# Performance work log

Measured on AMD Instinct MI355X. Metric: run time of the kernel, lower is better.

The kernel has to match this reference:

```python
import jax, jax.numpy as jnp
import numpy as np

B, C, H, L, P = 64, 64, 256, 64, 32
N_REAL = 2047
N = N_REAL + 1  # slot 0 is the null-child zero vector


def setup_inputs() -> dict:
    key = jax.random.key(0)
    ks = jax.random.split(key, 8)
    return {
        "node_feats": jax.random.normal(ks[0], (B, C, N), jnp.float32),
        "z": jax.random.normal(ks[1], (B, L), jnp.float32),
        "children": jax.random.randint(ks[2], (B, 3 * N_REAL), 0, N, jnp.int32),
        "conv1_w": jax.random.normal(ks[3], (H, C, 3), jnp.float32) * 0.05,
        "conv1_b": jnp.zeros((H,), jnp.float32),
        "conv2_w": jax.random.normal(ks[4], (H, H, 3), jnp.float32) * 0.05,
        "conv2_b": jnp.zeros((H,), jnp.float32),
        "mlp_w1": jax.random.normal(ks[5], (H + L, H), jnp.float32) * 0.05,
        "mlp_b1": jnp.zeros((H,), jnp.float32),
        "mlp_w2": jax.random.normal(ks[6], (H, P), jnp.float32) * 0.05,
        "mlp_b2": jnp.zeros((P,), jnp.float32),
    }


def _tree_conv(x, children, w, b):
    # x: [B, Cin, N]; children: [B, 3*N_real] indices of (self,left,right) triples
    g = jax.vmap(lambda xb, ib: xb[:, ib])(x, children)      # [B, Cin, 3*N_real]
    g = g.reshape(g.shape[0], g.shape[1], -1, 3)             # [B, Cin, N_real, 3]
    out = jnp.einsum('bcnk,hck->bhn', g, w) + b[None, :, None]  # Conv1d k=3 s=3
    zero = jnp.zeros((out.shape[0], out.shape[1], 1), out.dtype)
    return jnp.concatenate([zero, out], axis=2)              # [B, Cout, N]


def _tree_norm(x):
    # TreeLayerNorm: normalize each tree over all (channel, node) elements
    mean = jnp.mean(x, axis=(1, 2), keepdims=True)
    std = jnp.std(x, axis=(1, 2), keepdims=True, ddof=1)  # torch.std is unbiased
    return (x - mean) / (std + 1e-5)


def reference(node_feats, z, children, conv1_w, conv1_b, conv2_w, conv2_b,
              mlp_w1, mlp_b1, mlp_w2, mlp_b2):
    x = _tree_conv(node_feats, children, conv1_w, conv1_b)
    x = jax.nn.relu(_tree_norm(x))
    x = _tree_conv(x, children, conv2_w, conv2_b)
    x = jax.nn.relu(_tree_norm(x))                           # [B, H, N]
    z_exp = jnp.broadcast_to(z[:, :, None], (z.shape[0], z.shape[1], x.shape[2]))
    xz = jnp.concatenate([x, z_exp], axis=1)                 # [B, H+L, N]
    xz = xz.transpose(0, 2, 1)                               # [B, N, H+L]
    h = jax.nn.relu(xz @ mlp_w1 + mlp_b1)                    # [B, N, H]
    return h @ mlp_w2 + mlp_b2                               # [B, N, P]
```

## Files before the change

### kernel.cpp

```cpp
#include <hip/hip_runtime.h>
#include <hip/hip_bf16.h>

#define BATCH 64
#define CC    64
#define HH    256
#define LL    64
#define PP    32
#define NREAL 2047
#define NN    2048
#define MTOT  (HH*NN)

typedef unsigned short u16;
typedef __attribute__((ext_vector_type(8))) short short8;
typedef __attribute__((ext_vector_type(4))) float f32x4;

__device__ __forceinline__ float bu2f(u16 u) {
    return __uint_as_float(((unsigned)u) << 16);
}
__device__ __forceinline__ u16 f2bu(float f) {
    __hip_bfloat16 h = __float2bfloat16(f);
    return *reinterpret_cast<u16*>(&h);
}
__device__ __forceinline__ float ldv(const void* p, long long i, int f32) {
    return f32 ? ((const float*)p)[i] : bu2f(((const u16*)p)[i]);
}

__device__ __forceinline__ void swz(int id, int& b, int& tile) {
    b    = (id & 7) + 8 * ((id >> 3) & 7);
    tile = id >> 6;
}

__global__ __launch_bounds__(256) void detect_k(const u16* __restrict__ nf,
                                                int* __restrict__ flag) {
    __shared__ int cnt;
    if (threadIdx.x == 0) cnt = 0;
    __syncthreads();
    int c = 0;
#pragma unroll
    for (int i = 0; i < 16; ++i) {
        unsigned u = nf[threadIdx.x * 16 + i];
        unsigned e = (u >> 7) & 0xFF;
        if (e >= 161) c++;
    }
    atomicAdd(&cnt, c);
    __syncthreads();
    if (threadIdx.x == 0) flag[0] = (cnt > 64) ? 1 : 0;
}

__global__ __launch_bounds__(256) void prep_k(const void* __restrict__ c1w,
                                              const void* __restrict__ c2w,
                                              u16* __restrict__ wt1m,
                                              u16* __restrict__ wt2m,
                                              u16* __restrict__ x1t,
                                              float* __restrict__ statsz,
                                              const int* __restrict__ flag) {
    int isF32 = flag[0];
    int blk = blockIdx.x, tid = threadIdx.x;
    if (blk < 960) {
        const void* w = (blk < 192) ? c1w : c2w;
        u16* dst      = (blk < 192) ? wt1m : wt2m;
        int cinShift  = (blk < 192) ? 6 : 8;
        int t = ((blk < 192) ? blk : (blk - 192)) * 256 + tid;
        int CIN = 1 << cinShift;
        int kin = t & 31;
        int rest = t >> 5;
        int h = rest & (HH - 1);
        int ks = rest >> 8;
        int k = ks * 32 + kin;
        int kk = k >> cinShift, c = k & (CIN - 1);
        dst[t] = f2bu(ldv(w, (((long long)h << cinShift) + c) * 3 + kk, isF32));
    } else {
        int b = blk - 960;
        x1t[(long long)b * NN * HH + tid] = 0;
        if (b == 0) statsz[tid] = 0.f;
    }
}

__global__ __launch_bounds__(256) void tr_nf_k(const void* __restrict__ nf,
                                               u16* __restrict__ nf_t,
                                               const int* __restrict__ flag) {
    __shared__ u16 t[64][65];
    int isF32 = flag[0];
    int b = blockIdx.y;
    int n0 = blockIdx.x * 64;
    int tid = threadIdx.x;
    int lane = tid & 63, grp = tid >> 6;
#pragma unroll
    for (int i = 0; i < 16; ++i) {
        int c = grp * 16 + i;
        float v = ldv(nf, ((long long)b * CC + c) * NN + n0 + lane, isF32);
        t[c][lane] = f2bu(v);
    }
    __syncthreads();
#pragma unroll
    for (int i = 0; i < 16; ++i) {
        int n = grp * 16 + i;
        nf_t[((long long)b * NN + n0 + n) * CC + lane] = t[lane][n];
    }
}

__global__ __launch_bounds__(256) void wmlp2_k(const void* __restrict__ mw1,
                                               const void* __restrict__ mw2,
                                               u16* __restrict__ w1m,
                                               u16* __restrict__ w2m,
                                               const int* __restrict__ flag) {
    int isF32 = flag[0];
    int blk = blockIdx.x, tid = threadIdx.x;
    const void* w = (blk < 320) ? mw1 : mw2;
    u16* dst      = (blk < 320) ? w1m : w2m;
    int colShift  = (blk < 320) ? 8 : 5;
    int t = ((blk < 320) ? blk : (blk - 320)) * 256 + tid;
    int COLS = 1 << colShift;
    int kin = t & 31;
    int rest = t >> 5;
    int col = rest & (COLS - 1);
    int ks = rest >> colShift;
    dst[t] = f2bu(ldv(w, ((long long)(ks * 32 + kin) << colShift) + col, isF32));
}

__device__ __forceinline__ void load_norm(const float* stats, int b,
                                          float& mean, float& rstd) {
    float s = stats[b * 2], ss = stats[b * 2 + 1];
    float m = s / (float)MTOT;
    float var = (ss - s * s / (float)MTOT) / (float)(MTOT - 1);
    var = fmaxf(var, 0.f);
    mean = m;
    rstd = 1.f / (sqrtf(var) + 1e-5f);
}

template<int CIN>
__global__ __launch_bounds__(512, 2) void convm_k(const u16* __restrict__ x_t,
                                                  const int* __restrict__ children,
                                                  const u16* __restrict__ wtm,
                                                  const void* __restrict__ bias,
                                                  const float* __restrict__ stats_in,
                                                  float* __restrict__ stats_out,
                                                  u16* __restrict__ out_t,
                                                  const int* __restrict__ flag) {
    constexpr int KT = CIN / 32;
    constexpr int RE = CIN + 8;
    __shared__ u16 A[2][64 * RE];
    __shared__ int cidx[192];
    __shared__ float ps[16];

    int isF32 = flag[0];
    int b, ntile;
    swz(blockIdx.x, b, ntile);
    int n0 = ntile * 64;
    int tid = threadIdx.x;
    int lane = tid & 63, w = tid >> 6;
    int l15 = lane & 15, quad = lane >> 4;

    float mean = 0.f, rstd = 1.f;
    bool donorm = (stats_in != nullptr);
    if (donorm) load_norm(stats_in, b, mean, rstd);

    const long long cbase = (long long)b * (3 * NREAL);
    if (tid < 192) {
        int gi = 3 * n0 + tid;
        cidx[tid] = (gi < 3 * NREAL) ? children[cbase + gi] : 0;
    }
    __syncthreads();

    const long long xbase = (long long)b * NN;
    const u16* wb = wtm + ((long long)(w * 32 + l15)) * 32 + quad * 8;

    if (CIN == 256) {
        uint2 g0[8];
#pragma unroll
        for (int u = 0; u < 8; ++u) {
            int nd = w * 8 + u;
            g0[u] = *(const uint2*)(x_t + (xbase + cidx[3 * nd]) * CIN + lane * 4);
        }
#pragma unroll
        for (int u = 0; u < 8; ++u) {
            int nd = w * 8 + u;
            float f[4];
            f[0] = bu2f((u16)(g0[u].x & 0xffff)); f[1] = bu2f((u16)(g0[u].x >> 16));
            f[2] = bu2f((u16)(g0[u].y & 0xffff)); f[3] = bu2f((u16)(g0[u].y >> 16));
            if (donorm) {
#pragma unroll
                for (int j = 0; j < 4; ++j) f[j] = fmaxf((f[j] - mean) * rstd, 0.f);
            }
            uint2 o;
            o.x = (unsigned)f2bu(f[0]) | ((unsigned)f2bu(f[1]) << 16);
            o.y = (unsigned)f2bu(f[2]) | ((unsigned)f2bu(f[3]) << 16);
            *(uint2*)&A[0][nd * RE + lane * 4] = o;
        }
    } else {
        uint2 g0[2];
#pragma unroll
        for (int u = 0; u < 2; ++u) {
            int nd = w * 8 + u * 4 + quad;
            g0[u] = *(const uint2*)(x_t + (xbase + cidx[3 * nd]) * CIN + l15 * 4);
        }
#pragma unroll
        for (int u = 0; u < 2; ++u) {
            int nd = w * 8 + u * 4 + quad;
            *(uint2*)&A[0][nd * RE + l15 * 4] = g0[u];
        }
    }
    __syncthreads();

    f32x4 acc[4][2];
#pragma unroll
    for (int mt = 0; mt < 4; ++mt)
#pragma unroll
        for (int nt = 0; nt < 2; ++nt) acc[mt][nt] = (f32x4){0.f, 0.f, 0.f, 0.f};

#pragma unroll
    for (int t = 0; t < 3; ++t) {
        const u16* Ac = &A[t & 1][0];
        u16* An = &A[(t + 1) & 1][0];

        short8 Bc[KT][2];
#pragma unroll
        for (int ks = 0; ks < KT; ++ks) {
            const u16* wn = wb + (long long)(t * KT + ks) * 8192;
            Bc[ks][0] = *(const short8*)(wn);
            Bc[ks][1] = *(const short8*)(wn + 512);
        }

        uint2 gv[8];
        uint2 gs[2];
        if (t < 2) {
            if (CIN == 256) {
#pragma unroll
                for (int u = 0; u < 8; ++u) {
                    int nd = w * 8 + u;
                    gv[u] = *(const uint2*)(x_t + (xbase + cidx[3 * nd + t + 1]) * CIN
                                            + lane * 4);
                }
            } else {
#pragma unroll
                for (int u = 0; u < 2; ++u) {
                    int nd = w * 8 + u * 4 + quad;
                    gs[u] = *(const uint2*)(x_t + (xbase + cidx[3 * nd + t + 1]) * CIN
                                            + l15 * 4);
                }
            }
        }

        short8 a0 = *(const short8*)&Ac[(l15)      * RE + quad * 8];
        short8 a1 = *(const short8*)&Ac[(16 + l15) * RE + quad * 8];
        short8 a2 = *(const short8*)&Ac[(32 + l15) * RE + quad * 8];
        short8 a3 = *(const short8*)&Ac[(48 + l15) * RE + quad * 8];
#pragma unroll
        for (int ks = 0; ks < KT; ++ks) {
            short8 ca0 = a0, ca1 = a1, ca2 = a2, ca3 = a3;
            if (ks + 1 < KT) {
                int ko = (ks + 1) * 32 + quad * 8;
                a0 = *(const short8*)&Ac[(l15)      * RE + ko];
                a1 = *(const short8*)&Ac[(16 + l15) * RE + ko];
                a2 = *(const short8*)&Ac[(32 + l15) * RE + ko];
                a3 = *(const short8*)&Ac[(48 + l15) * RE + ko];
            }
            acc[0][0] = __builtin_amdgcn_mfma_f32_16x16x32_bf16(ca0, Bc[ks][0], acc[0][0], 0, 0, 0);
            acc[1][0] = __builtin_amdgcn_mfma_f32_16x16x32_bf16(ca1, Bc[ks][0], acc[1][0], 0, 0, 0);
            acc[2][0] = __builtin_amdgcn_mfma_f32_16x16x32_bf16(ca2, Bc[ks][0], acc[2][0], 0, 0, 0);
            acc[3][0] = __builtin_amdgcn_mfma_f32_16x16x32_bf16(ca3, Bc[ks][0], acc[3][0], 0, 0, 0);
            acc[0][1] = __builtin_amdgcn_mfma_f32_16x16x32_bf16(ca0, Bc[ks][1], acc[0][1], 0, 0, 0);
            acc[1][1] = __builtin_amdgcn_mfma_f32_16x16x32_bf16(ca1, Bc[ks][1], acc[1][1], 0, 0, 0);
            acc[2][1] = __builtin_amdgcn_mfma_f32_16x16x32_bf16(ca2, Bc[ks][1], acc[2][1], 0, 0, 0);
            acc[3][1] = __builtin_amdgcn_mfma_f32_16x16x32_bf16(ca3, Bc[ks][1], acc[3][1], 0, 0, 0);
        }

        if (t < 2) {
            if (CIN == 256) {
#pragma unroll
                for (int u = 0; u < 8; ++u) {
                    int nd = w * 8 + u;
                    float f[4];
                    f[0] = bu2f((u16)(gv[u].x & 0xffff));
                    f[1] = bu2f((u16)(gv[u].x >> 16));
                    f[2] = bu2f((u16)(gv[u].y & 0xffff));
                    f[3] = bu2f((u16)(gv[u].y >> 16));
                    if (donorm) {
#pragma unroll
                        for (int j = 0; j < 4; ++j)
                            f[j] = fmaxf((f[j] - mean) * rstd, 0.f);
                    }
                    uint2 o;
                    o.x = (unsigned)f2bu(f[0]) | ((unsigned)f2bu(f[1]) << 16);
                    o.y = (unsigned)f2bu(f[2]) | ((unsigned)f2bu(f[3]) << 16);
                    *(uint2*)&An[nd * RE + lane * 4] = o;
                }
            } else {
#pragma unroll
                for (int u = 0; u < 2; ++u) {
                    int nd = w * 8 + u * 4 + quad;
                    *(uint2*)&An[nd * RE + l15 * 4] = gs[u];
                }
            }
        }
        __syncthreads();
    }

    float s = 0.f, ss = 0.f;
#pragma unroll
    for (int nt = 0; nt < 2; ++nt) {
        int h = w * 32 + nt * 16 + l15;
        float bv = ldv(bias, h, isF32);
#pragma unroll
        for (int mt = 0; mt < 4; ++mt) {
#pragma unroll
            for (int r = 0; r < 4; ++r) {
                int nc = n0 + mt * 16 + quad * 4 + r;
                if (nc < NREAL) {
                    float v = acc[mt][nt][r] + bv;
                    s += v;
                    ss += v * v;
                    out_t[((long long)b * NN + 1 + nc) * HH + h] = f2bu(v);
                }
            }
        }
    }
#pragma unroll
    for (int off = 32; off; off >>= 1) {
        s  += __shfl_down(s, off);
        ss += __shfl_down(ss, off);
    }
    if (lane == 0) { ps[w] = s; ps[8 + w] = ss; }
    __syncthreads();
    if (tid == 0) {
        float S = 0.f, SS = 0.f;
#pragma unroll
        for (int i = 0; i < 8; ++i) { S += ps[i]; SS += ps[8 + i]; }
        atomicAdd(&stats_out[b * 2],     S);
        atomicAdd(&stats_out[b * 2 + 1], SS);
    }
    if (CIN == 256 && ntile == 0 && tid < 32) {
        uint4 zz = {0u, 0u, 0u, 0u};
        *(uint4*)&out_t[((long long)b * NN) * HH + tid * 8] = zz;
    }
}

#define REX 328
#define REH 264
__global__ __launch_bounds__(256, 4) void mlpm_k(const u16* __restrict__ x2t,
                                                 const void* __restrict__ z,
                                                 const u16* __restrict__ w1m,
                                                 const void* __restrict__ b1,
                                                 const u16* __restrict__ w2m,
                                                 const void* __restrict__ b2,
                                                 const float* __restrict__ stats,
                                                 void* __restrict__ out,
                                                 const int* __restrict__ flag) {
    __shared__ u16 xz[32 * REX];
    __shared__ u16 hbuf[32 * REH];
    int isF32 = flag[0];
    int b, tile;
    swz(blockIdx.x, b, tile);
    int n0 = tile * 32;
    int tid = threadIdx.x;
    int lane = tid & 63, w = tid >> 6;
    int l15 = lane & 15, quad = lane >> 4;

    float mean, rstd;
    load_norm(stats, b, mean, rstd);
    u16 zb = f2bu(ldv(z, (long long)b * LL + lane, isF32));

    uint2 vv[8];
#pragma unroll
    for (int u = 0; u < 8; ++u) {
        int node = w * 8 + u;
        vv[u] = *(const uint2*)(x2t + ((long long)(b * NN + n0 + node)) * HH
                                + lane * 4);
    }
#pragma unroll
    for (int u = 0; u < 8; ++u) {
        int node = w * 8 + u;
        float f[4];
        f[0] = bu2f((u16)(vv[u].x & 0xffff));
        f[1] = bu2f((u16)(vv[u].x >> 16));
        f[2] = bu2f((u16)(vv[u].y & 0xffff));
        f[3] = bu2f((u16)(vv[u].y >> 16));
#pragma unroll
        for (int j = 0; j < 4; ++j) f[j] = fmaxf((f[j] - mean) * rstd, 0.f);
        uint2 o;
        o.x = (unsigned)f2bu(f[0]) | ((unsigned)f2bu(f[1]) << 16);
        o.y = (unsigned)f2bu(f[2]) | ((unsigned)f2bu(f[3]) << 16);
        *(uint2*)&xz[node * REX + lane * 4] = o;
        xz[node * REX + HH + lane] = zb;
    }
    __syncthreads();

    f32x4 acc[2][4];
#pragma unroll
    for (int mt = 0; mt < 2; ++mt)
#pragma unroll
        for (int nt = 0; nt < 4; ++nt) acc[mt][nt] = (f32x4){0.f, 0.f, 0.f, 0.f};

    const u16* wbase = w1m + ((long long)(w * 64 + l15)) * 32 + quad * 8;
    short8 bf0 = *(const short8*)(wbase);
    short8 bf1 = *(const short8*)(wbase + 512);
    short8 bf2 = *(const short8*)(wbase + 1024);
    short8 bf3 = *(const short8*)(wbase + 1536);
    short8 a0 = *(const short8*)&xz[l15 * REX + quad * 8];
    short8 a1 = *(const short8*)&xz[(16 + l15) * REX + quad * 8];

    for (int ks = 0; ks < 10; ++ks) {
        short8 c0 = bf0, c1 = bf1, c2 = bf2, c3 = bf3;
        short8 ca0 = a0, ca1 = a1;
        if (ks + 1 < 10) {
            const u16* wn = wbase + (long long)(ks + 1) * 8192;
            bf0 = *(const short8*)(wn);
            bf1 = *(const short8*)(wn + 512);
            bf2 = *(const short8*)(wn + 1024);
            bf3 = *(const short8*)(wn + 1536);
            a0 = *(const short8*)&xz[l15 * REX + (ks + 1) * 32 + quad * 8];
            a1 = *(const short8*)&xz[(16 + l15) * REX + (ks + 1) * 32 + quad * 8];
        }
        acc[0][0] = __builtin_amdgcn_mfma_f32_16x16x32_bf16(ca0, c0, acc[0][0], 0, 0, 0);
        acc[1][0] = __builtin_amdgcn_mfma_f32_16x16x32_bf16(ca1, c0, acc[1][0], 0, 0, 0);
        acc[0][1] = __builtin_amdgcn_mfma_f32_16x16x32_bf16(ca0, c1, acc[0][1], 0, 0, 0);
        acc[1][1] = __builtin_amdgcn_mfma_f32_16x16x32_bf16(ca1, c1, acc[1][1], 0, 0, 0);
        acc[0][2] = __builtin_amdgcn_mfma_f32_16x16x32_bf16(ca0, c2, acc[0][2], 0, 0, 0);
        acc[1][2] = __builtin_amdgcn_mfma_f32_16x16x32_bf16(ca1, c2, acc[1][2], 0, 0, 0);
        acc[0][3] = __builtin_amdgcn_mfma_f32_16x16x32_bf16(ca0, c3, acc[0][3], 0, 0, 0);
        acc[1][3] = __builtin_amdgcn_mfma_f32_16x16x32_bf16(ca1, c3, acc[1][3], 0, 0, 0);
    }
#pragma unroll
    for (int nt = 0; nt < 4; ++nt) {
        int j = w * 64 + nt * 16 + l15;
        float bv = ldv(b1, j, isF32);
#pragma unroll
        for (int mt = 0; mt < 2; ++mt)
#pragma unroll
            for (int r = 0; r < 4; ++r) {
                int node = mt * 16 + quad * 4 + r;
                hbuf[node * REH + j] = f2bu(fmaxf(acc[mt][nt][r] + bv, 0.f));
            }
    }
    __syncthreads();

    int mt = w & 1, nt = w >> 1;
    f32x4 acc2 = (f32x4){0.f, 0.f, 0.f, 0.f};
#pragma unroll
    for (int ks = 0; ks < 8; ++ks) {
        short8 a = *(const short8*)&hbuf[(mt * 16 + l15) * REH + ks * 32 + quad * 8];
        short8 bf = *(const short8*)(w2m + ((long long)ks * PP + nt * 16 + l15) * 32 + quad * 8);
        acc2 = __builtin_amdgcn_mfma_f32_16x16x32_bf16(a, bf, acc2, 0, 0, 0);
    }
    int p = nt * 16 + l15;
    float bp = ldv(b2, p, isF32);
#pragma unroll
    for (int r = 0; r < 4; ++r) {
        int node = mt * 16 + quad * 4 + r;
        long long o = ((long long)(b * NN + n0 + node)) * PP + p;
        float v = acc2[r] + bp;
        if (isF32) ((float*)out)[o] = v;
        else       ((u16*)out)[o] = f2bu(v);
    }
}

__global__ __launch_bounds__(256) void fill0_k(void* out, const int* flag, int n) {
    int i = blockIdx.x * 256 + threadIdx.x;
    if (i >= n) return;
    if (flag[0]) ((float*)out)[i] = 0.f;
    else ((u16*)out)[i] = 0;
}

extern "C" void kernel_launch(void* const* d_in, const int* in_sizes, int n_in,
                              void* d_out, int out_size, void* d_ws, size_t ws_size,
                              hipStream_t stream) {
    const void* nf  = d_in[0];
    const void* z   = d_in[1];
    const int*  ch  = (const int*)d_in[2];
    const void* c1w = d_in[3];
    const void* c1b = d_in[4];
    const void* c2w = d_in[5];
    const void* c2b = d_in[6];
    const void* mw1 = d_in[7];
    const void* mb1 = d_in[8];
    const void* mw2 = d_in[9];
    const void* mb2 = d_in[10];

    char* ws = (char*)d_ws;
    int*   flag   = (int*)ws;
    float* statsz = (float*)(ws + 256);
    float* stats1 = (float*)(ws + 256);
    float* stats2 = (float*)(ws + 768);
    u16* x1t  = (u16*)(ws + 4096);
    u16* A    = (u16*)(ws + 4096 + 67108864LL);
    u16* nf_t = A;
    u16* x2t  = A;
    u16* wt1m = (u16*)d_out;
    u16* wt2m = wt1m + 192 * 256;
    u16* w1m = x1t;
    u16* w2m = x1t + 320 * 256;

    const size_t NEED = 4096 + 2 * 67108864ULL;
    if (ws_size < NEED) {
        detect_k<<<1, 256, 0, stream>>>((const u16*)nf, flag);
        fill0_k<<<(out_size + 255) / 256, 256, 0, stream>>>(d_out, flag, out_size);
        return;
    }

    detect_k<<<1, 256, 0, stream>>>((const u16*)nf, flag);
    prep_k<<<1024, 256, 0, stream>>>(c1w, c2w, wt1m, wt2m, x1t, statsz, flag);
    tr_nf_k<<<dim3(NN / 64, BATCH), 256, 0, stream>>>(nf, nf_t, flag);

    convm_k<CC><<<32 * BATCH, 512, 0, stream>>>(nf_t, ch, wt1m, c1b,
                                                nullptr, stats1, x1t, flag);
    convm_k<HH><<<32 * BATCH, 512, 0, stream>>>(x1t, ch, wt2m, c2b,
                                                stats1, stats2, x2t, flag);
    wmlp2_k<<<352, 256, 0, stream>>>(mw1, mw2, w1m, w2m, flag);
    mlpm_k<<<64 * BATCH, 256, 0, stream>>>(x2t, z, w1m, mb1, w2m, mb2,
                                           stats2, d_out, flag);
}
```

Measured before the change: 301.4 us.

## Split conv kernels, use async global-to-LDS gather for conv1, widen MLP loads

Replaces the templated conv kernel with a dedicated conv1 kernel. It gathers all three child taps up front into a swizzled LDS buffer using global_load_lds async copies, then runs a single 6-step MFMA loop instead of the three-tap double-buffered pipeline. conv2 is specialized to CIN=256 with the normalization always applied. The MLP kernel now loads node features with 16-byte vector loads. s_setprio is raised around the MFMA loops. The async-copy path depends on the swizzle addressing and per-lane LDS placement being correct, and conv1's LDS footprint grows.

```diff
diff --git a/kernel.cpp b/kernel.cpp
--- a/kernel.cpp
+++ b/kernel.cpp
@@ -23,6 +23,13 @@
 }
 __device__ __forceinline__ float ldv(const void* p, long long i, int f32) {
     return f32 ? ((const float*)p)[i] : bu2f(((const u16*)p)[i]);
+}
+
+__device__ __forceinline__ void async_cp16(const u16* src, u16* dst) {
+    __builtin_amdgcn_global_load_lds(
+        (const __attribute__((address_space(1))) unsigned int*)src,
+        (__attribute__((address_space(3))) unsigned int*)dst,
+        16, 0, 0);
 }
 
 __device__ __forceinline__ void swz(int id, int& b, int& tile) {
@@ -128,8 +135,129 @@
     rstd = 1.f / (sqrtf(var) + 1e-5f);
 }
 
-template<int CIN>
-__global__ __launch_bounds__(512, 2) void convm_k(const u16* __restrict__ x_t,
+__global__ __launch_bounds__(512, 2) void conv1_k(const u16* __restrict__ x_t,
+                                                  const int* __restrict__ children,
+                                                  const u16* __restrict__ wtm,
+                                                  const void* __restrict__ bias,
+                                                  float* __restrict__ stats_out,
+                                                  u16* __restrict__ out_t,
+                                                  const int* __restrict__ flag) {
+    __shared__ u16 S[192 * CC];
+    __shared__ int cidx[192];
+    __shared__ float ps[16];
+
+    int isF32 = flag[0];
+    int b, ntile;
+    swz(blockIdx.x, b, ntile);
+    int n0 = ntile * 64;
+    int tid = threadIdx.x;
+    int lane = tid & 63, w = tid >> 6;
+    int l15 = lane & 15, quad = lane >> 4;
+
+    const long long cbase = (long long)b * (3 * NREAL);
+    if (tid < 192) {
+        int gi = 3 * n0 + tid;
+        cidx[tid] = (gi < 3 * NREAL) ? children[cbase + gi] : 0;
+    }
+    __syncthreads();
+
+    const long long xbase = (long long)b * NN;
+    const u16* wb = wtm + ((long long)(w * 32 + l15)) * 32 + quad * 8;
+
+    {
+        int li = lane & 7;
+#pragma unroll
+        for (int g = 0; g < 3; ++g) {
+            int rbase = w * 24 + g * 8;
+            int r = rbase + (lane >> 3);
+            int tap = r >> 6, nd = r & 63;
+            int ci = cidx[3 * nd + tap];
+            const u16* src = x_t + (xbase + ci) * CC
+                             + ((li * 8) ^ ((r & 7) << 3));
+            async_cp16(src, &S[rbase * CC]);
+        }
+    }
+    __syncthreads();
+
+    f32x4 acc[4][2];
+#pragma unroll
+    for (int mt = 0; mt < 4; ++mt) {
+        acc[mt][0] = (f32x4){0.f, 0.f, 0.f, 0.f};
+        acc[mt][1] = (f32x4){0.f, 0.f, 0.f, 0.f};
+    }
+    const int X = (l15 & 7) << 3;
+
+    auto ard = [&](int ksg, int mt) -> short8 {
+        int tap = ksg >> 1;
+        int col = (ksg & 1) * 32 + quad * 8;
+        int r = tap * 64 + mt * 16 + l15;
+        return *(const short8*)&S[r * CC + (col ^ X)];
+    };
+
+    short8 b0 = *(const short8*)(wb);
+    short8 b1 = *(const short8*)(wb + 512);
+    short8 a[4];
+#pragma unroll
+    for (int mt = 0; mt < 4; ++mt) a[mt] = ard(0, mt);
+
+    __builtin_amdgcn_s_setprio(1);
+#pragma unroll
+    for (int ksg = 0; ksg < 6; ++ksg) {
+        short8 cb0 = b0, cb1 = b1;
+        short8 ca[4];
+#pragma unroll
+        for (int mt = 0; mt < 4; ++mt) ca[mt] = a[mt];
+        if (ksg + 1 < 6) {
+            const u16* wn = wb + (long long)(ksg + 1) * 8192;
+            b0 = *(const short8*)(wn);
+            b1 = *(const short8*)(wn + 512);
+#pragma unroll
+            for (int mt = 0; mt < 4; ++mt) a[mt] = ard(ksg + 1, mt);
+        }
+#pragma unroll
+        for (int mt = 0; mt < 4; ++mt) {
+            acc[mt][0] = __builtin_amdgcn_mfma_f32_16x16x32_bf16(ca[mt], cb0, acc[mt][0], 0, 0, 0);
+            acc[mt][1] = __builtin_amdgcn_mfma_f32_16x16x32_bf16(ca[mt], cb1, acc[mt][1], 0, 0, 0);
+        }
+    }
+    __builtin_amdgcn_s_setprio(0);
+
+    float s = 0.f, ss = 0.f;
+#pragma unroll
+    for (int nt = 0; nt < 2; ++nt) {
+        int h = w * 32 + nt * 16 + l15;
+        float bv = ldv(bias, h, isF32);
+#pragma unroll
+        for (int mt = 0; mt < 4; ++mt) {
+#pragma unroll
+            for (int r = 0; r < 4; ++r) {
+                int nc = n0 + mt * 16 + quad * 4 + r;
+                if (nc < NREAL) {
+                    float v = acc[mt][nt][r] + bv;
+                    s += v;
+                    ss += v * v;
+                    out_t[((long long)b * NN + 1 + nc) * HH + h] = f2bu(v);
+                }
+            }
+        }
+    }
+#pragma unroll
+    for (int off = 32; off; off >>= 1) {
+        s  += __shfl_down(s, off);
+        ss += __shfl_down(ss, off);
+    }
+    if (lane == 0) { ps[w] = s; ps[8 + w] = ss; }
+    __syncthreads();
+    if (tid == 0) {
+        float S_ = 0.f, SS_ = 0.f;
+#pragma unroll
+        for (int i = 0; i < 8; ++i) { S_ += ps[i]; SS_ += ps[8 + i]; }
+        atomicAdd(&stats_out[b * 2],     S_);
+        atomicAdd(&stats_out[b * 2 + 1], SS_);
+    }
+}
+
+__global__ __launch_bounds__(512, 2) void conv2_k(const u16* __restrict__ x_t,
                                                   const int* __restrict__ children,
                                                   const u16* __restrict__ wtm,
                                                   const void* __restrict__ bias,
@@ -137,8 +265,8 @@
                                                   float* __restrict__ stats_out,
                                                   u16* __restrict__ out_t,
                                                   const int* __restrict__ flag) {
-    constexpr int KT = CIN / 32;
-    constexpr int RE = CIN + 8;
+    constexpr int KT = 8;
+    constexpr int RE = HH + 8;
     __shared__ u16 A[2][64 * RE];
     __shared__ int cidx[192];
     __shared__ float ps[16];
@@ -151,9 +279,8 @@
     int lane = tid & 63, w = tid >> 6;
     int l15 = lane & 15, quad = lane >> 4;
 
-    float mean = 0.f, rstd = 1.f;
-    bool donorm = (stats_in != nullptr);
-    if (donorm) load_norm(stats_in, b, mean, rstd);
+    float mean, rstd;
+    load_norm(stats_in, b, mean, rstd);
 
     const long long cbase = (long long)b * (3 * NREAL);
     if (tid < 192) {
@@ -165,12 +292,12 @@
     const long long xbase = (long long)b * NN;
     const u16* wb = wtm + ((long long)(w * 32 + l15)) * 32 + quad * 8;
 
-    if (CIN == 256) {
+    {
         uint2 g0[8];
 #pragma unroll
         for (int u = 0; u < 8; ++u) {
             int nd = w * 8 + u;
-            g0[u] = *(const uint2*)(x_t + (xbase + cidx[3 * nd]) * CIN + lane * 4);
+            g0[u] = *(const uint2*)(x_t + (xbase + cidx[3 * nd]) * HH + lane * 4);
         }
 #pragma unroll
         for (int u = 0; u < 8; ++u) {
@@ -178,27 +305,13 @@
             float f[4];
             f[0] = bu2f((u16)(g0[u].x & 0xffff)); f[1] = bu2f((u16)(g0[u].x >> 16));
             f[2] = bu2f((u16)(g0[u].y & 0xffff)); f[3] = bu2f((u16)(g0[u].y >> 16));
-            if (donorm) {
-#pragma unroll
-                for (int j = 0; j < 4; ++j) f[j] = fmaxf((f[j] - mean) * rstd, 0.f);
-            }
+#pragma unroll
+            for (int j = 0; j < 4; ++j) f[j] = fmaxf((f[j] - mean) * rstd, 0.f);
             uint2 o;
             o.x = (unsigned)f2bu(f[0]) | ((unsigned)f2bu(f[1]) << 16);
             o.y = (unsigned)f2bu(f[2]) | ((unsigned)f2bu(f[3]) << 16);
             *(uint2*)&A[0][nd * RE + lane * 4] = o;
         }
-    } else {
-        uint2 g0[2];
-#pragma unroll
-        for (int u = 0; u < 2; ++u) {
-            int nd = w * 8 + u * 4 + quad;
-            g0[u] = *(const uint2*)(x_t + (xbase + cidx[3 * nd]) * CIN + l15 * 4);
-        }
-#pragma unroll
-        for (int u = 0; u < 2; ++u) {
-            int nd = w * 8 + u * 4 + quad;
-            *(uint2*)&A[0][nd * RE + l15 * 4] = g0[u];
-        }
     }
     __syncthreads();
 
@@ -222,22 +335,12 @@
         }
 
         uint2 gv[8];
-        uint2 gs[2];
         if (t < 2) {
-            if (CIN == 256) {
-#pragma unroll
-                for (int u = 0; u < 8; ++u) {
-                    int nd = w * 8 + u;
-                    gv[u] = *(const uint2*)(x_t + (xbase + cidx[3 * nd + t + 1]) * CIN
-                                            + lane * 4);
-                }
-            } else {
-#pragma unroll
-                for (int u = 0; u < 2; ++u) {
-                    int nd = w * 8 + u * 4 + quad;
-                    gs[u] = *(const uint2*)(x_t + (xbase + cidx[3 * nd + t + 1]) * CIN
-                                            + l15 * 4);
-                }
+#pragma unroll
+            for (int u = 0; u < 8; ++u) {
+                int nd = w * 8 + u;
+                gv[u] = *(const uint2*)(x_t + (xbase + cidx[3 * nd + t + 1]) * HH
+                                        + lane * 4);
             }
         }
 
@@ -245,6 +348,7 @@
         short8 a1 = *(const short8*)&Ac[(16 + l15) * RE + quad * 8];
         short8 a2 = *(const short8*)&Ac[(32 + l15) * RE + quad * 8];
         short8 a3 = *(const short8*)&Ac[(48 + l15) * RE + quad * 8];
+        __builtin_amdgcn_s_setprio(1);
 #pragma unroll
         for (int ks = 0; ks < KT; ++ks) {
             short8 ca0 = a0, ca1 = a1, ca2 = a2, ca3 = a3;
@@ -264,33 +368,24 @@
             acc[2][1] = __builtin_amdgcn_mfma_f32_16x16x32_bf16(ca2, Bc[ks][1], acc[2][1], 0, 0, 0);
             acc[3][1] = __builtin_amdgcn_mfma_f32_16x16x32_bf16(ca3, Bc[ks][1], acc[3][1], 0, 0, 0);
         }
+        __builtin_amdgcn_s_setprio(0);
 
         if (t < 2) {
-            if (CIN == 256) {
-#pragma unroll
-                for (int u = 0; u < 8; ++u) {
-                    int nd = w * 8 + u;
-                    float f[4];
-                    f[0] = bu2f((u16)(gv[u].x & 0xffff));
-                    f[1] = bu2f((u16)(gv[u].x >> 16));
-                    f[2] = bu2f((u16)(gv[u].y & 0xffff));
-                    f[3] = bu2f((u16)(gv[u].y >> 16));
-                    if (donorm) {
-#pragma unroll
-                        for (int j = 0; j < 4; ++j)
-                            f[j] = fmaxf((f[j] - mean) * rstd, 0.f);
-                    }
-                    uint2 o;
-                    o.x = (unsigned)f2bu(f[0]) | ((unsigned)f2bu(f[1]) << 16);
-                    o.y = (unsigned)f2bu(f[2]) | ((unsigned)f2bu(f[3]) << 16);
-                    *(uint2*)&An[nd * RE + lane * 4] = o;
-                }
-            } else {
-#pragma unroll
-                for (int u = 0; u < 2; ++u) {
-                    int nd = w * 8 + u * 4 + quad;
-                    *(uint2*)&An[nd * RE + l15 * 4] = gs[u];
-                }
+#pragma unroll
+            for (int u = 0; u < 8; ++u) {
+                int nd = w * 8 + u;
+                float f[4];
+                f[0] = bu2f((u16)(gv[u].x & 0xffff));
+                f[1] = bu2f((u16)(gv[u].x >> 16));
+                f[2] = bu2f((u16)(gv[u].y & 0xffff));
+                f[3] = bu2f((u16)(gv[u].y >> 16));
+#pragma unroll
+                for (int j = 0; j < 4; ++j)
+                    f[j] = fmaxf((f[j] - mean) * rstd, 0.f);
+                uint2 o;
+                o.x = (unsigned)f2bu(f[0]) | ((unsigned)f2bu(f[1]) << 16);
+                o.y = (unsigned)f2bu(f[2]) | ((unsigned)f2bu(f[3]) << 16);
+                *(uint2*)&An[nd * RE + lane * 4] = o;
             }
         }
         __syncthreads();
@@ -323,13 +418,13 @@
     if (lane == 0) { ps[w] = s; ps[8 + w] = ss; }
     __syncthreads();
     if (tid == 0) {
-        float S = 0.f, SS = 0.f;
-#pragma unroll
-        for (int i = 0; i < 8; ++i) { S += ps[i]; SS += ps[8 + i]; }
-        atomicAdd(&stats_out[b * 2],     S);
-        atomicAdd(&stats_out[b * 2 + 1], SS);
-    }
-    if (CIN == 256 && ntile == 0 && tid < 32) {
+        float S_ = 0.f, SS_ = 0.f;
+#pragma unroll
+        for (int i = 0; i < 8; ++i) { S_ += ps[i]; SS_ += ps[8 + i]; }
+        atomicAdd(&stats_out[b * 2],     S_);
+        atomicAdd(&stats_out[b * 2 + 1], SS_);
+    }
+    if (ntile == 0 && tid < 32) {
         uint4 zz = {0u, 0u, 0u, 0u};
         *(uint4*)&out_t[((long long)b * NN) * HH + tid * 8] = zz;
     }
@@ -360,29 +455,30 @@
     load_norm(stats, b, mean, rstd);
     u16 zb = f2bu(ldv(z, (long long)b * LL + lane, isF32));
 
-    uint2 vv[8];
-#pragma unroll
-    for (int u = 0; u < 8; ++u) {
-        int node = w * 8 + u;
-        vv[u] = *(const uint2*)(x2t + ((long long)(b * NN + n0 + node)) * HH
-                                + lane * 4);
-    }
-#pragma unroll
-    for (int u = 0; u < 8; ++u) {
-        int node = w * 8 + u;
-        float f[4];
-        f[0] = bu2f((u16)(vv[u].x & 0xffff));
-        f[1] = bu2f((u16)(vv[u].x >> 16));
-        f[2] = bu2f((u16)(vv[u].y & 0xffff));
-        f[3] = bu2f((u16)(vv[u].y >> 16));
-#pragma unroll
-        for (int j = 0; j < 4; ++j) f[j] = fmaxf((f[j] - mean) * rstd, 0.f);
-        uint2 o;
-        o.x = (unsigned)f2bu(f[0]) | ((unsigned)f2bu(f[1]) << 16);
-        o.y = (unsigned)f2bu(f[2]) | ((unsigned)f2bu(f[3]) << 16);
-        *(uint2*)&xz[node * REX + lane * 4] = o;
-        xz[node * REX + HH + lane] = zb;
-    }
+    uint4 vv[4];
+#pragma unroll
+    for (int u = 0; u < 4; ++u) {
+        int node = w * 8 + u * 2 + (lane >> 5);
+        int lo = lane & 31;
+        vv[u] = *(const uint4*)(x2t + ((long long)(b * NN + n0 + node)) * HH
+                                + lo * 8);
+    }
+#pragma unroll
+    for (int u = 0; u < 4; ++u) {
+        int node = w * 8 + u * 2 + (lane >> 5);
+        int lo = lane & 31;
+        unsigned wd[4] = {vv[u].x, vv[u].y, vv[u].z, vv[u].w};
+#pragma unroll
+        for (int j = 0; j < 4; ++j) {
+            float flo = fmaxf((bu2f((u16)(wd[j] & 0xffff)) - mean) * rstd, 0.f);
+            float fhi = fmaxf((bu2f((u16)(wd[j] >> 16))   - mean) * rstd, 0.f);
+            wd[j] = (unsigned)f2bu(flo) | ((unsigned)f2bu(fhi) << 16);
+        }
+        *(uint4*)&xz[node * REX + lo * 8] = make_uint4(wd[0], wd[1], wd[2], wd[3]);
+    }
+#pragma unroll
+    for (int u = 0; u < 8; ++u)
+        xz[(w * 8 + u) * REX + HH + lane] = zb;
     __syncthreads();
 
     f32x4 acc[2][4];
@@ -399,6 +495,7 @@
     short8 a0 = *(const short8*)&xz[l15 * REX + quad * 8];
     short8 a1 = *(const short8*)&xz[(16 + l15) * REX + quad * 8];
 
+    __builtin_amdgcn_s_setprio(1);
     for (int ks = 0; ks < 10; ++ks) {
         short8 c0 = bf0, c1 = bf1, c2 = bf2, c3 = bf3;
         short8 ca0 = a0, ca1 = a1;
@@ -420,6 +517,7 @@
         acc[0][3] = __builtin_amdgcn_mfma_f32_16x16x32_bf16(ca0, c3, acc[0][3], 0, 0, 0);
         acc[1][3] = __builtin_amdgcn_mfma_f32_16x16x32_bf16(ca1, c3, acc[1][3], 0, 0, 0);
     }
+    __builtin_amdgcn_s_setprio(0);
 #pragma unroll
     for (int nt = 0; nt < 4; ++nt) {
         int j = w * 64 + nt * 16 + l15;
@@ -501,10 +599,10 @@
     prep_k<<<1024, 256, 0, stream>>>(c1w, c2w, wt1m, wt2m, x1t, statsz, flag);
     tr_nf_k<<<dim3(NN / 64, BATCH), 256, 0, stream>>>(nf, nf_t, flag);
 
-    convm_k<CC><<<32 * BATCH, 512, 0, stream>>>(nf_t, ch, wt1m, c1b,
-                                                nullptr, stats1, x1t, flag);
-    convm_k<HH><<<32 * BATCH, 512, 0, stream>>>(x1t, ch, wt2m, c2b,
-                                                stats1, stats2, x2t, flag);
+    conv1_k<<<32 * BATCH, 512, 0, stream>>>(nf_t, ch, wt1m, c1b,
+                                            stats1, x1t, flag);
+    conv2_k<<<32 * BATCH, 512, 0, stream>>>(x1t, ch, wt2m, c2b,
+                                            stats1, stats2, x2t, flag);
     wmlp2_k<<<352, 256, 0, stream>>>(mw1, mw2, w1m, w2m, flag);
     mlpm_k<<<64 * BATCH, 256, 0, stream>>>(x2t, z, w1m, mb1, w2m, mb2,
                                            stats2, d_out, flag);
```

Result: slower. 323.5 us (+7.3%).
